# Kernel tuning notes

Hardware: AMD Instinct MI355X
Metric: run time of the kernel (lower is better)

Reference implementation:

```python
import jax, jax.numpy as jnp
import numpy as np

N, E, B = 100000, 3200000, 512
D_IN, D_H, HID = 500, 64, 200
NUM_CLASSES = 80
EPS_BN = 1e-5


def _sage(x, src, dst, Wl, bl, Wr):
    # PyG SAGEConv (mean aggr): out = lin_l(mean_{j->i} x_j) + lin_r(x_i)
    n = x.shape[0]
    agg = jax.ops.segment_sum(x[src], dst, num_segments=n)          # [n, d_in]
    deg = jax.ops.segment_sum(jnp.ones((src.shape[0],), x.dtype), dst, num_segments=n)
    mean = agg / jnp.maximum(deg, 1.0)[:, None]
    return mean @ Wl + bl + x @ Wr


def _bn(c, g, b):
    # BatchNorm1d, training-mode batch statistics (biased var)
    mu = c.mean(0)
    var = c.var(0)
    return (c - mu) / jnp.sqrt(var + EPS_BN) * g + b


def setup_inputs() -> dict:
    key = jax.random.key(0)
    ks = jax.random.split(key, 16)
    p = lambda k, shape: jax.random.normal(k, shape, dtype=jnp.float32) * 0.05
    z = lambda d: jnp.zeros((d,), jnp.float32)
    o = lambda d: jnp.ones((d,), jnp.float32)
    return {
        "x": jax.random.uniform(ks[0], (N, D_IN), dtype=jnp.float32),
        "edge_index": jax.random.randint(ks[1], (2, E), 0, N),
        "batch": jnp.sort(jax.random.randint(ks[2], (N,), 0, B)),
        "y": jax.random.randint(ks[3], (B,), 0, NUM_CLASSES),
        "conv1_Wl": p(ks[4], (D_IN, D_H)), "conv1_bl": z(D_H), "conv1_Wr": p(ks[5], (D_IN, D_H)),
        "conv2_Wl": p(ks[6], (D_H, D_H)),  "conv2_bl": z(D_H), "conv2_Wr": p(ks[7], (D_H, D_H)),
        "conv3_Wl": p(ks[8], (D_H, D_H)),  "conv3_bl": z(D_H), "conv3_Wr": p(ks[9], (D_H, D_H)),
        "lin1_W": p(ks[10], (D_H, HID)), "lin1_b": z(HID),
        "bn1_g": o(HID), "bn1_beta": z(HID),
        "lin2_W": p(ks[11], (HID, HID // 2)), "lin2_b": z(HID // 2),
        "bn2_g": o(HID // 2), "bn2_beta": z(HID // 2),
        "lin3_W": p(ks[12], (HID // 2, HID // 2)), "lin3_b": z(HID // 2),
        "bn3_g": o(HID // 2), "bn3_beta": z(HID // 2),
        "lin4_W": p(ks[13], (HID // 2, NUM_CLASSES)), "lin4_b": z(NUM_CLASSES),
    }


def reference(x, edge_index, batch, y,
              conv1_Wl, conv1_bl, conv1_Wr,
              conv2_Wl, conv2_bl, conv2_Wr,
              conv3_Wl, conv3_bl, conv3_Wr,
              lin1_W, lin1_b, bn1_g, bn1_beta,
              lin2_W, lin2_b, bn2_g, bn2_beta,
              lin3_W, lin3_b, bn3_g, bn3_beta,
              lin4_W, lin4_b):
    src, dst = edge_index[0], edge_index[1]
    # F.normalize(x, p=1.0, dim=-1)
    xn = x / jnp.maximum(jnp.abs(x).sum(-1, keepdims=True), 1e-12)
    e = _sage(xn, src, dst, conv1_Wl, conv1_bl, conv1_Wr)
    e = _sage(e, src, dst, conv2_Wl, conv2_bl, conv2_Wr)
    e = _sage(e, src, dst, conv3_Wl, conv3_bl, conv3_Wr)
    # global_mean_pool over graph ids
    sums = jax.ops.segment_sum(e, batch, num_segments=B)             # [B, 64]
    cnts = jax.ops.segment_sum(jnp.ones((e.shape[0],), e.dtype), batch, num_segments=B)
    c = sums / jnp.maximum(cnts, 1.0)[:, None]
    # dropout (p=0.1) omitted for a deterministic reference
    c = c @ lin1_W + lin1_b
    b = jnp.tanh(_bn(c, bn1_g, bn1_beta))
    c = b @ lin2_W + lin2_b
    b = jnp.tanh(_bn(c, bn2_g, bn2_beta))
    c = b @ lin3_W + lin3_b
    b = jnp.tanh(_bn(c, bn3_g, bn3_beta))
    return b @ lin4_W + lin4_b                                       # [B, 80]
```

## Files before the change

### kernel.cpp

```cpp
#include <hip/hip_runtime.h>
#include <hip/hip_bf16.h>

#define NN 100000
#define NE 3200000
#define NB 512
#define DIN 500
#define DH 64
#define HIDN 200
#define NCLS 80

#define NBUK 256
#define NPB 391
#define EPB 16384
#define NBLK_E ((NE + EPB - 1) / EPB)

typedef __attribute__((ext_vector_type(8))) short bf16x8;
typedef __attribute__((ext_vector_type(4))) float f32x4;

__device__ __forceinline__ short f2bf(float f) {
    union { float f; unsigned u; } v; v.f = f;
    unsigned r = v.u + 0x7FFF + ((v.u >> 16) & 1);
    return (short)(r >> 16);
}
__device__ __forceinline__ float bf2f(short s) {
    union { unsigned u; float f; } v; v.u = ((unsigned)(unsigned short)s) << 16;
    return v.f;
}

__global__ void bukhist_kernel(const int* __restrict__ dst, int* __restrict__ block_hist) {
    __shared__ int h[NBUK];
    for (int i = threadIdx.x; i < NBUK; i += 256) h[i] = 0;
    __syncthreads();
    int base = blockIdx.x * EPB;
    int end = min(base + EPB, NE);
    for (int e = base + threadIdx.x; e < end; e += 256)
        atomicAdd(&h[dst[e] / NPB], 1);
    __syncthreads();
    for (int i = threadIdx.x; i < NBUK; i += 256)
        block_hist[blockIdx.x * NBUK + i] = h[i];
}

__global__ void bukoff_kernel(int* __restrict__ block_hist, int* __restrict__ buk_base) {
    __shared__ int tot[NBUK];
    __shared__ int sc[NBUK];
    int b = threadIdx.x;
    int s = 0;
    for (int i = 0; i < NBLK_E; ++i) s += block_hist[i * NBUK + b];
    tot[b] = s; sc[b] = s;
    __syncthreads();
    for (int o = 1; o < NBUK; o <<= 1) {
        int t = (b >= o) ? sc[b - o] : 0;
        __syncthreads();
        sc[b] += t;
        __syncthreads();
    }
    int excl = sc[b] - tot[b];
    buk_base[b] = excl;
    if (b == NBUK - 1) buk_base[NBUK] = excl + tot[b];
    int run = excl;
    for (int i = 0; i < NBLK_E; ++i) {
        int idx = i * NBUK + b;
        int v = block_hist[idx];
        block_hist[idx] = run;
        run += v;
    }
}

__global__ void bukscat_kernel(const int* __restrict__ src, const int* __restrict__ dst,
                               const int* __restrict__ block_hist, int* __restrict__ bpack) {
    __shared__ int cur[NBUK];
    for (int i = threadIdx.x; i < NBUK; i += 256)
        cur[i] = block_hist[blockIdx.x * NBUK + i];
    __syncthreads();
    int base = blockIdx.x * EPB;
    int end = min(base + EPB, NE);
    for (int e = base + threadIdx.x; e < end; e += 256) {
        int d = dst[e];
        int bk = d / NPB;
        int p = atomicAdd(&cur[bk], 1);
        bpack[p] = (src[e] << 9) | (d - bk * NPB);
    }
}

__global__ void bukfin_kernel(const int* __restrict__ buk_base, const int* __restrict__ bpack,
                              int* __restrict__ row_ptr, float* __restrict__ invdeg,
                              int* __restrict__ csr_src) {
    __shared__ int cnt[NPB];
    __shared__ int cbase[NPB];
    int bk = blockIdx.x;
    int n0 = bk * NPB;
    int nloc = min(n0 + NPB, NN) - n0;
    for (int i = threadIdx.x; i < nloc; i += 256) cnt[i] = 0;
    __syncthreads();
    int beg = buk_base[bk], end = buk_base[bk + 1];
    for (int p = beg + threadIdx.x; p < end; p += 256)
        atomicAdd(&cnt[bpack[p] & 511], 1);
    __syncthreads();
    if (threadIdx.x == 0) {
        int run = beg;
        for (int i = 0; i < nloc; ++i) { int v = cnt[i]; cbase[i] = run; run += v; }
    }
    __syncthreads();
    for (int i = threadIdx.x; i < nloc; i += 256) {
        row_ptr[n0 + i] = cbase[i];
        invdeg[n0 + i] = 1.0f / fmaxf((float)cnt[i], 1.0f);
        cnt[i] = cbase[i];
    }
    if (bk == NBUK - 1 && threadIdx.x == 0) row_ptr[NN] = end;
    __syncthreads();
    for (int p = beg + threadIdx.x; p < end; p += 256) {
        int v = bpack[p];
        int q = atomicAdd(&cnt[v & 511], 1);
        csr_src[q] = v >> 9;
    }
}

__global__ void wprep_frag(const float* __restrict__ Wl, const float* __restrict__ Wr,
                           short* __restrict__ Wf) {
    int id = blockIdx.x * blockDim.x + threadIdx.x;
    if (id >= 16 * 8 * 64) return;
    int l = id & 63;
    int c = (id >> 6) & 7;
    int t = id >> 9;
    int q = l >> 4, r16 = l & 15;
    int col = c * 16 + r16;
    short v[8];
#pragma unroll
    for (int i = 0; i < 8; ++i) {
        int k = t * 32 + q * 8 + i;
        float f = 0.f;
        if (k < DIN) f = (col < 64) ? Wl[(size_t)k * 64 + col] : Wr[(size_t)k * 64 + (col - 64)];
        v[i] = f2bf(f);
    }
    *(bf16x8*)(Wf + (size_t)id * 8) = *(bf16x8*)v;
}

__global__ void wprep64(const float* __restrict__ W, short* __restrict__ Wb) {
    int id = blockIdx.x * blockDim.x + threadIdx.x;
    if (id >= 64 * 64) return;
    int col = id >> 6, k = id & 63;
    Wb[col * 64 + k] = f2bf(W[(size_t)k * 64 + col]);
}

__launch_bounds__(256)
__global__ void gemm_direct2(const float* __restrict__ in, const short* __restrict__ Wf,
                             short* __restrict__ Hl, float* __restrict__ Hr) {
    const int tid = threadIdx.x;
    const int w = tid >> 6, l = tid & 63;
    const int q = l >> 4, r16 = l & 15;
    const int tile0 = blockIdx.x * 64 + w * 16;
    const int arow_i = tile0 + r16;
    const bool ok = arow_i < NN;
    const float* arow = in + (size_t)(ok ? arow_i : 0) * DIN + q * 8;
    const short* wf = Wf + (size_t)l * 8;

    f32x4 acc[8];
#pragma unroll
    for (int c = 0; c < 8; ++c) acc[c] = (f32x4){0.f, 0.f, 0.f, 0.f};
    float pabs = 0.f;

#pragma unroll 2
    for (int t = 0; t < 16; ++t) {
        float v[8];
        if (t < 15) {
            const float4 f0 = *(const float4*)(arow + t * 32);
            const float4 f1 = *(const float4*)(arow + t * 32 + 4);
            v[0] = f0.x; v[1] = f0.y; v[2] = f0.z; v[3] = f0.w;
            v[4] = f1.x; v[5] = f1.y; v[6] = f1.z; v[7] = f1.w;
        } else {
#pragma unroll
            for (int i = 0; i < 8; ++i) {
                int gk = t * 32 + q * 8 + i;
                v[i] = (gk < DIN) ? arow[t * 32 + i] : 0.f;
            }
        }
        short sh[8];
#pragma unroll
        for (int i = 0; i < 8; ++i) { pabs += fabsf(v[i]); sh[i] = f2bf(v[i]); }
        bf16x8 a = *(bf16x8*)sh;
#pragma unroll
        for (int c = 0; c < 8; ++c) {
            bf16x8 b = *(const bf16x8*)(wf + ((size_t)(t * 8 + c) << 9));
            acc[c] = __builtin_amdgcn_mfma_f32_16x16x32_bf16(a, b, acc[c], 0, 0, 0);
        }
    }

    pabs += __shfl_xor(pabs, 16, 64);
    pabs += __shfl_xor(pabs, 32, 64);
    float sval = 1.0f / fmaxf(pabs, 1e-12f);

#pragma unroll
    for (int rr = 0; rr < 4; ++rr) {
        int lrow = q * 4 + rr;
        float srow = __shfl(sval, lrow, 64);
        int grow = tile0 + lrow;
        if (grow < NN) {
#pragma unroll
            for (int c = 0; c < 8; ++c) {
                float o = acc[c][rr] * srow;
                if (c < 4) Hl[(size_t)grow * 64 + c * 16 + r16] = f2bf(o);
                else       Hr[(size_t)grow * 64 + (c - 4) * 16 + r16] = o;
            }
        }
    }
}

__launch_bounds__(256)
__global__ void gather_kernel(const int* __restrict__ row_ptr, const int* __restrict__ csr_src,
                              const short* __restrict__ Hl, const float* __restrict__ Hr,
                              const float* __restrict__ invdeg, const float* __restrict__ bl,
                              short* __restrict__ ebf) {
    int node = blockIdx.x * 4 + (threadIdx.x >> 6);
    if (node >= NN) return;
    int lane = threadIdx.x & 63;
    int ng = lane >> 3;
    int fl = lane & 7;
    int beg = row_ptr[node], end = row_ptr[node + 1];
    float a0[8], a1[8];
#pragma unroll
    for (int j = 0; j < 8; ++j) { a0[j] = 0.f; a1[j] = 0.f; }
    int p = beg + ng;
    for (; p + 8 < end; p += 16) {
        int s0 = csr_src[p];
        int s1 = csr_src[p + 8];
        bf16x8 v0 = *(const bf16x8*)(Hl + (size_t)s0 * 64 + fl * 8);
        bf16x8 v1 = *(const bf16x8*)(Hl + (size_t)s1 * 64 + fl * 8);
#pragma unroll
        for (int j = 0; j < 8; ++j) { a0[j] += bf2f(v0[j]); a1[j] += bf2f(v1[j]); }
    }
    if (p < end) {
        int s0 = csr_src[p];
        bf16x8 v0 = *(const bf16x8*)(Hl + (size_t)s0 * 64 + fl * 8);
#pragma unroll
        for (int j = 0; j < 8; ++j) a0[j] += bf2f(v0[j]);
    }
#pragma unroll
    for (int j = 0; j < 8; ++j) a0[j] += a1[j];
#pragma unroll
    for (int m = 8; m < 64; m <<= 1)
#pragma unroll
        for (int j = 0; j < 8; ++j) a0[j] += __shfl_xor(a0[j], m, 64);
    if (ng == 0) {
        float idg = invdeg[node];
        const float4 h0 = *(const float4*)(Hr + (size_t)node * 64 + fl * 8);
        const float4 h1 = *(const float4*)(Hr + (size_t)node * 64 + fl * 8 + 4);
        short s[8];
        s[0] = f2bf(a0[0] * idg + bl[fl * 8 + 0] + h0.x);
        s[1] = f2bf(a0[1] * idg + bl[fl * 8 + 1] + h0.y);
        s[2] = f2bf(a0[2] * idg + bl[fl * 8 + 2] + h0.z);
        s[3] = f2bf(a0[3] * idg + bl[fl * 8 + 3] + h0.w);
        s[4] = f2bf(a0[4] * idg + bl[fl * 8 + 4] + h1.x);
        s[5] = f2bf(a0[5] * idg + bl[fl * 8 + 5] + h1.y);
        s[6] = f2bf(a0[6] * idg + bl[fl * 8 + 6] + h1.z);
        s[7] = f2bf(a0[7] * idg + bl[fl * 8 + 7] + h1.w);
        *(bf16x8*)(ebf + (size_t)node * 64 + fl * 8) = *(bf16x8*)s;
    }
}

__launch_bounds__(256)
__global__ void gathermean_kernel(const int* __restrict__ row_ptr, const int* __restrict__ csr_src,
                                  const short* __restrict__ ein, const float* __restrict__ invdeg,
                                  short* __restrict__ m) {
    int node = blockIdx.x * 4 + (threadIdx.x >> 6);
    if (node >= NN) return;
    int lane = threadIdx.x & 63;
    int ng = lane >> 3;
    int fl = lane & 7;
    int beg = row_ptr[node], end = row_ptr[node + 1];
    float a0[8], a1[8];
#pragma unroll
    for (int j = 0; j < 8; ++j) { a0[j] = 0.f; a1[j] = 0.f; }
    int p = beg + ng;
    for (; p + 8 < end; p += 16) {
        int s0 = csr_src[p];
        int s1 = csr_src[p + 8];
        bf16x8 v0 = *(const bf16x8*)(ein + (size_t)s0 * 64 + fl * 8);
        bf16x8 v1 = *(const bf16x8*)(ein + (size_t)s1 * 64 + fl * 8);
#pragma unroll
        for (int j = 0; j < 8; ++j) { a0[j] += bf2f(v0[j]); a1[j] += bf2f(v1[j]); }
    }
    if (p < end) {
        int s0 = csr_src[p];
        bf16x8 v0 = *(const bf16x8*)(ein + (size_t)s0 * 64 + fl * 8);
#pragma unroll
        for (int j = 0; j < 8; ++j) a0[j] += bf2f(v0[j]);
    }
#pragma unroll
    for (int j = 0; j < 8; ++j) a0[j] += a1[j];
#pragma unroll
    for (int mm = 8; mm < 64; mm <<= 1)
#pragma unroll
        for (int j = 0; j < 8; ++j) a0[j] += __shfl_xor(a0[j], mm, 64);
    if (ng == 0) {
        float idg = invdeg[node];
        short s[8];
#pragma unroll
        for (int j = 0; j < 8; ++j) s[j] = f2bf(a0[j] * idg);
        *(bf16x8*)(m + (size_t)node * 64 + fl * 8) = *(bf16x8*)s;
    }
}

template<bool LAST>
__launch_bounds__(256)
__global__ void gemm_dual64(const short* __restrict__ m, const short* __restrict__ ein,
                            const short* __restrict__ Wbl, const short* __restrict__ Wbr,
                            const float* __restrict__ bl,
                            short* __restrict__ eout, float* __restrict__ e3out) {
    const int tid = threadIdx.x;
    const int row0 = blockIdx.x * 64;
    const int w = tid >> 6, l = tid & 63;
    const int q = l >> 4, r16 = l & 15;
    const int arow = row0 + w * 16 + r16;
    const bool ok = arow < NN;
    const short* mp = m   + (size_t)(ok ? arow : 0) * 64 + q * 8;
    const short* ep = ein + (size_t)(ok ? arow : 0) * 64 + q * 8;
    f32x4 acc[4];
#pragma unroll
    for (int c = 0; c < 4; ++c) acc[c] = (f32x4){0.f, 0.f, 0.f, 0.f};
    const bf16x8 z8 = (bf16x8){0, 0, 0, 0, 0, 0, 0, 0};
#pragma unroll
    for (int t = 0; t < 2; ++t) {
        bf16x8 am = ok ? *(const bf16x8*)(mp + t * 32) : z8;
        bf16x8 ae = ok ? *(const bf16x8*)(ep + t * 32) : z8;
#pragma unroll
        for (int c = 0; c < 4; ++c) {
            bf16x8 wl = *(const bf16x8*)(Wbl + (size_t)(c * 16 + r16) * 64 + t * 32 + q * 8);
            bf16x8 wr = *(const bf16x8*)(Wbr + (size_t)(c * 16 + r16) * 64 + t * 32 + q * 8);
            acc[c] = __builtin_amdgcn_mfma_f32_16x16x32_bf16(am, wl, acc[c], 0, 0, 0);
            acc[c] = __builtin_amdgcn_mfma_f32_16x16x32_bf16(ae, wr, acc[c], 0, 0, 0);
        }
    }
#pragma unroll
    for (int c = 0; c < 4; ++c) {
#pragma unroll
        for (int rr = 0; rr < 4; ++rr) {
            int grow = row0 + w * 16 + q * 4 + rr;
            int col = c * 16 + r16;
            if (grow < NN) {
                float o = acc[c][rr] + bl[col];
                if (LAST) e3out[(size_t)grow * 64 + col] = o;
                else      eout[(size_t)grow * 64 + col]  = f2bf(o);
            }
        }
    }
}

__global__ void gseg_kernel(const int* __restrict__ batch, int* __restrict__ gstart) {
    int i = blockIdx.x * blockDim.x + threadIdx.x;
    if (i >= NN) return;
    int bc = batch[i];
    int bp = (i == 0) ? -1 : batch[i - 1];
    for (int b = bp + 1; b <= bc; ++b) gstart[b] = i;
    if (i == NN - 1)
        for (int b = bc + 1; b <= NB; ++b) gstart[b] = NN;
}

__launch_bounds__(256)
__global__ void pool_seg(const float* __restrict__ e, const int* __restrict__ gstart,
                         float* __restrict__ c0) {
    __shared__ float part[4][64];
    int b = blockIdx.x;
    int w = threadIdx.x >> 6, lane = threadIdx.x & 63;
    int s = gstart[b], t = gstart[b + 1];
    float acc = 0.f;
    for (int i = s + w; i < t; i += 4) acc += e[(size_t)i * 64 + lane];
    part[w][lane] = acc;
    __syncthreads();
    if (w == 0) {
        float v = part[0][lane] + part[1][lane] + part[2][lane] + part[3][lane];
        c0[b * 64 + lane] = v / fmaxf((float)(t - s), 1.0f);
    }
}

__global__ void lin_kernel(const float* __restrict__ in, const float* __restrict__ W,
                           const float* __restrict__ bias, float* __restrict__ out,
                           int Kd, int Dout) {
    int id = blockIdx.x * blockDim.x + threadIdx.x;
    if (id >= NB * Dout) return;
    int row = id / Dout, col = id - row * Dout;
    const float* ir = in + (size_t)row * Kd;
    float acc = bias[col];
    for (int k = 0; k < Kd; ++k) acc += ir[k] * W[(size_t)k * Dout + col];
    out[id] = acc;
}

__global__ void bnstats_kernel(const float* __restrict__ c, const float* __restrict__ g,
                               const float* __restrict__ beta, float* __restrict__ sa,
                               float* __restrict__ sb, int Dout) {
    int col = blockIdx.x;
    int tid = threadIdx.x;
    float s = 0.f, sq = 0.f;
    for (int r = tid; r < NB; r += 256) {
        float v = c[(size_t)r * Dout + col];
        s += v; sq += v * v;
    }
    __shared__ float ls[256], lq[256];
    ls[tid] = s; lq[tid] = sq;
    __syncthreads();
    for (int o = 128; o > 0; o >>= 1) {
        if (tid < o) { ls[tid] += ls[tid + o]; lq[tid] += lq[tid + o]; }
        __syncthreads();
    }
    if (tid == 0) {
        float mu = ls[0] / NB;
        float var = lq[0] / NB - mu * mu;
        float a = g[col] * rsqrtf(var + 1e-5f);
        sa[col] = a;
        sb[col] = beta[col] - mu * a;
    }
}

__global__ void bnapply_kernel(const float* __restrict__ c, const float* __restrict__ sa,
                               const float* __restrict__ sb, float* __restrict__ bv, int Dout) {
    int id = blockIdx.x * blockDim.x + threadIdx.x;
    if (id >= NB * Dout) return;
    int col = id % Dout;
    bv[id] = tanhf(c[id] * sa[col] + sb[col]);
}

extern "C" void kernel_launch(void* const* d_in, const int* in_sizes, int n_in,
                              void* d_out, int out_size, void* d_ws, size_t ws_size,
                              hipStream_t stream) {
    const float* x    = (const float*)d_in[0];
    const int* ei     = (const int*)d_in[1];
    const int* src    = ei;
    const int* dst    = ei + NE;
    const int* batch  = (const int*)d_in[2];
    const float* c1Wl = (const float*)d_in[4];
    const float* c1bl = (const float*)d_in[5];
    const float* c1Wr = (const float*)d_in[6];
    const float* c2Wl = (const float*)d_in[7];
    const float* c2bl = (const float*)d_in[8];
    const float* c2Wr = (const float*)d_in[9];
    const float* c3Wl = (const float*)d_in[10];
    const float* c3bl = (const float*)d_in[11];
    const float* c3Wr = (const float*)d_in[12];
    const float* l1W  = (const float*)d_in[13]; const float* l1b = (const float*)d_in[14];
    const float* bn1g = (const float*)d_in[15]; const float* bn1b = (const float*)d_in[16];
    const float* l2W  = (const float*)d_in[17]; const float* l2b = (const float*)d_in[18];
    const float* bn2g = (const float*)d_in[19]; const float* bn2b = (const float*)d_in[20];
    const float* l3W  = (const float*)d_in[21]; const float* l3b = (const float*)d_in[22];
    const float* bn3g = (const float*)d_in[23]; const float* bn3b = (const float*)d_in[24];
    const float* l4W  = (const float*)d_in[25]; const float* l4b = (const float*)d_in[26];
    float* out = (float*)d_out;

    char* wsb = (char*)d_ws;
    short* Hl     = (short*)wsb; wsb += (size_t)NN * 64 * 2;
    float* Hr     = (float*)wsb; wsb += (size_t)NN * 64 * 4;
    short* e      = (short*)wsb; wsb += (size_t)NN * 64 * 2;
    short* m      = (short*)wsb; wsb += (size_t)NN * 64 * 2;
    float* e3     = (float*)wsb; wsb += (size_t)NN * 64 * 4;
    float* invdeg = (float*)wsb; wsb += (size_t)NN * 4;
    float* c      = (float*)wsb; wsb += (size_t)NB * HIDN * 4;
    float* bv     = (float*)wsb; wsb += (size_t)NB * HIDN * 4;
    float* sa     = (float*)wsb; wsb += HIDN * 4;
    float* sb     = (float*)wsb; wsb += HIDN * 4;
    short* Wf1    = (short*)wsb; wsb += 16 * 8 * 64 * 8 * 2;
    short* Wb2l   = (short*)wsb; wsb += 64 * 64 * 2;
    short* Wb2r   = (short*)wsb; wsb += 64 * 64 * 2;
    short* Wb3l   = (short*)wsb; wsb += 64 * 64 * 2;
    short* Wb3r   = (short*)wsb; wsb += 64 * 64 * 2;
    int* row_ptr  = (int*)wsb;   wsb += (size_t)(NN + 1) * 4;
    int* csr_src  = (int*)wsb;   wsb += (size_t)NE * 4;
    int* buk_base = (int*)wsb;   wsb += (NBUK + 1) * 4;
    int* gstart   = (int*)wsb;   wsb += (NB + 1) * 4;
    int* bpack      = (int*)Hl;
    int* block_hist = (int*)e;

    bukhist_kernel<<<NBLK_E, 256, 0, stream>>>(dst, block_hist);
    bukoff_kernel<<<1, NBUK, 0, stream>>>(block_hist, buk_base);
    bukscat_kernel<<<NBLK_E, 256, 0, stream>>>(src, dst, block_hist, bpack);
    bukfin_kernel<<<NBUK, 256, 0, stream>>>(buk_base, bpack, row_ptr, invdeg, csr_src);

    gseg_kernel<<<(NN + 255) / 256, 256, 0, stream>>>(batch, gstart);

    wprep_frag<<<(16 * 8 * 64 + 255) / 256, 256, 0, stream>>>(c1Wl, c1Wr, Wf1);
    wprep64<<<(64 * 64 + 255) / 256, 256, 0, stream>>>(c2Wl, Wb2l);
    wprep64<<<(64 * 64 + 255) / 256, 256, 0, stream>>>(c2Wr, Wb2r);
    wprep64<<<(64 * 64 + 255) / 256, 256, 0, stream>>>(c3Wl, Wb3l);
    wprep64<<<(64 * 64 + 255) / 256, 256, 0, stream>>>(c3Wr, Wb3r);

    const int GB64 = (NN + 63) / 64;
    const int GGB  = (NN + 3) / 4;

    gemm_direct2<<<GB64, 256, 0, stream>>>(x, Wf1, Hl, Hr);
    gather_kernel<<<GGB, 256, 0, stream>>>(row_ptr, csr_src, Hl, Hr, invdeg, c1bl, e);
    gathermean_kernel<<<GGB, 256, 0, stream>>>(row_ptr, csr_src, e, invdeg, m);
    gemm_dual64<false><<<GB64, 256, 0, stream>>>(m, e, Wb2l, Wb2r, c2bl, e, nullptr);
    gathermean_kernel<<<GGB, 256, 0, stream>>>(row_ptr, csr_src, e, invdeg, m);
    gemm_dual64<true><<<GB64, 256, 0, stream>>>(m, e, Wb3l, Wb3r, c3bl, nullptr, e3);

    pool_seg<<<NB, 256, 0, stream>>>(e3, gstart, bv);

    lin_kernel<<<(NB * 200 + 255) / 256, 256, 0, stream>>>(bv, l1W, l1b, c, 64, 200);
    bnstats_kernel<<<200, 256, 0, stream>>>(c, bn1g, bn1b, sa, sb, 200);
    bnapply_kernel<<<(NB * 200 + 255) / 256, 256, 0, stream>>>(c, sa, sb, bv, 200);

    lin_kernel<<<(NB * 100 + 255) / 256, 256, 0, stream>>>(bv, l2W, l2b, c, 200, 100);
    bnstats_kernel<<<100, 256, 0, stream>>>(c, bn2g, bn2b, sa, sb, 100);
    bnapply_kernel<<<(NB * 100 + 255) / 256, 256, 0, stream>>>(c, sa, sb, bv, 100);

    lin_kernel<<<(NB * 100 + 255) / 256, 256, 0, stream>>>(bv, l3W, l3b, c, 100, 100);
    bnstats_kernel<<<100, 256, 0, stream>>>(c, bn3g, bn3b, sa, sb, 100);
    bnapply_kernel<<<(NB * 100 + 255) / 256, 256, 0, stream>>>(c, sa, sb, bv, 100);

    lin_kernel<<<(NB * 80 + 255) / 256, 256, 0, stream>>>(bv, l4W, l4b, out, 100, 80);
}
```

Measured before the change: 613.6 us.

## Split first-layer GEMM K dimension across wave pairs with LDS reduction

The first SAGE projection GEMM now splits the 500-wide K dimension in half between two waves per 16-row tile, with each block covering 32 rows instead of 64. The second half's partial accumulators and L1-norm sums are reduced through shared memory before the scaled outputs are written. This halves each wave's serial MFMA/load chain and doubles the block count to expose more memory-level parallelism. In exchange it adds a __syncthreads, LDS traffic, and leaves half the waves idle during the epilogue.

```diff
diff --git a/kernel.cpp b/kernel.cpp
--- a/kernel.cpp
+++ b/kernel.cpp
@@ -143,16 +143,19 @@
 }
 
 __launch_bounds__(256)
-__global__ void gemm_direct2(const float* __restrict__ in, const short* __restrict__ Wf,
-                             short* __restrict__ Hl, float* __restrict__ Hr) {
+__global__ void gemm_splitk(const float* __restrict__ in, const short* __restrict__ Wf,
+                            short* __restrict__ Hl, float* __restrict__ Hr) {
+    __shared__ float red[2][64][36];
     const int tid = threadIdx.x;
     const int w = tid >> 6, l = tid & 63;
+    const int g = w >> 1;
+    const int h = w & 1;
     const int q = l >> 4, r16 = l & 15;
-    const int tile0 = blockIdx.x * 64 + w * 16;
+    const int tile0 = blockIdx.x * 32 + g * 16;
     const int arow_i = tile0 + r16;
     const bool ok = arow_i < NN;
-    const float* arow = in + (size_t)(ok ? arow_i : 0) * DIN + q * 8;
-    const short* wf = Wf + (size_t)l * 8;
+    const float* arow = in + (size_t)(ok ? arow_i : 0) * DIN + h * 256 + q * 8;
+    const short* wf = Wf + (size_t)l * 8 + (size_t)h * 8 * 8 * 512;
 
     f32x4 acc[8];
 #pragma unroll
@@ -160,9 +163,9 @@
     float pabs = 0.f;
 
 #pragma unroll 2
-    for (int t = 0; t < 16; ++t) {
+    for (int t = 0; t < 8; ++t) {
         float v[8];
-        if (t < 15) {
+        if (h == 0 || t < 7) {
             const float4 f0 = *(const float4*)(arow + t * 32);
             const float4 f1 = *(const float4*)(arow + t * 32 + 4);
             v[0] = f0.x; v[1] = f0.y; v[2] = f0.z; v[3] = f0.w;
@@ -170,7 +173,7 @@
         } else {
 #pragma unroll
             for (int i = 0; i < 8; ++i) {
-                int gk = t * 32 + q * 8 + i;
+                int gk = 256 + t * 32 + q * 8 + i;
                 v[i] = (gk < DIN) ? arow[t * 32 + i] : 0.f;
             }
         }
@@ -185,21 +188,34 @@
         }
     }
 
-    pabs += __shfl_xor(pabs, 16, 64);
-    pabs += __shfl_xor(pabs, 32, 64);
-    float sval = 1.0f / fmaxf(pabs, 1e-12f);
-
-#pragma unroll
-    for (int rr = 0; rr < 4; ++rr) {
-        int lrow = q * 4 + rr;
-        float srow = __shfl(sval, lrow, 64);
-        int grow = tile0 + lrow;
-        if (grow < NN) {
-#pragma unroll
-            for (int c = 0; c < 8; ++c) {
-                float o = acc[c][rr] * srow;
-                if (c < 4) Hl[(size_t)grow * 64 + c * 16 + r16] = f2bf(o);
-                else       Hr[(size_t)grow * 64 + (c - 4) * 16 + r16] = o;
+    if (h == 1) {
+#pragma unroll
+        for (int c = 0; c < 8; ++c) *(f32x4*)&red[g][l][c * 4] = acc[c];
+        red[g][l][32] = pabs;
+    }
+    __syncthreads();
+    if (h == 0) {
+#pragma unroll
+        for (int c = 0; c < 8; ++c) {
+            f32x4 o = *(f32x4*)&red[g][l][c * 4];
+            acc[c][0] += o[0]; acc[c][1] += o[1]; acc[c][2] += o[2]; acc[c][3] += o[3];
+        }
+        pabs += red[g][l][32];
+        pabs += __shfl_xor(pabs, 16, 64);
+        pabs += __shfl_xor(pabs, 32, 64);
+        float sval = 1.0f / fmaxf(pabs, 1e-12f);
+#pragma unroll
+        for (int rr = 0; rr < 4; ++rr) {
+            int lrow = q * 4 + rr;
+            float srow = __shfl(sval, lrow, 64);
+            int grow = tile0 + lrow;
+            if (grow < NN) {
+#pragma unroll
+                for (int c = 0; c < 8; ++c) {
+                    float o = acc[c][rr] * srow;
+                    if (c < 4) Hl[(size_t)grow * 64 + c * 16 + r16] = f2bf(o);
+                    else       Hr[(size_t)grow * 64 + (c - 4) * 16 + r16] = o;
+                }
             }
         }
     }
@@ -480,10 +496,11 @@
     wprep64<<<(64 * 64 + 255) / 256, 256, 0, stream>>>(c3Wl, Wb3l);
     wprep64<<<(64 * 64 + 255) / 256, 256, 0, stream>>>(c3Wr, Wb3r);
 
+    const int GB32 = (NN + 31) / 32;
     const int GB64 = (NN + 63) / 64;
     const int GGB  = (NN + 3) / 4;
 
-    gemm_direct2<<<GB64, 256, 0, stream>>>(x, Wf1, Hl, Hr);
+    gemm_splitk<<<GB32, 256, 0, stream>>>(x, Wf1, Hl, Hr);
     gather_kernel<<<GGB, 256, 0, stream>>>(row_ptr, csr_src, Hl, Hr, invdeg, c1bl, e);
     gathermean_kernel<<<GGB, 256, 0, stream>>>(row_ptr, csr_src, e, invdeg, m);
     gemm_dual64<false><<<GB64, 256, 0, stream>>>(m, e, Wb2l, Wb2r, c2bl, e, nullptr);
```

Result: faster. 601.4 us (-2.0%).

## Stage layer-1 weights through double-buffered LDS and software-pipeline input loads

Applied to the files above, without the earlier changes.

The first SAGE GEMM now loads the bf16 weight slice for each K-step cooperatively into a double-buffered LDS tile, and each wave reads its fragments from there. Before, every wave read its fragments straight from global memory. The x row loads for the next K-step are issued before the current MFMAs run, so global latency overlaps with compute. The weight prep kernel now writes a plain column-major padded layout to suit the LDS staging. The cost is LDS usage and a block-wide barrier at every K-step.

```diff
diff --git a/kernel.cpp b/kernel.cpp
--- a/kernel.cpp
+++ b/kernel.cpp
@@ -115,24 +115,14 @@
     }
 }
 
-__global__ void wprep_frag(const float* __restrict__ Wl, const float* __restrict__ Wr,
-                           short* __restrict__ Wf) {
+__global__ void wprep_kernel(const float* __restrict__ Wl, const float* __restrict__ Wr,
+                             short* __restrict__ Wb, int K, int KP) {
     int id = blockIdx.x * blockDim.x + threadIdx.x;
-    if (id >= 16 * 8 * 64) return;
-    int l = id & 63;
-    int c = (id >> 6) & 7;
-    int t = id >> 9;
-    int q = l >> 4, r16 = l & 15;
-    int col = c * 16 + r16;
-    short v[8];
-#pragma unroll
-    for (int i = 0; i < 8; ++i) {
-        int k = t * 32 + q * 8 + i;
-        float f = 0.f;
-        if (k < DIN) f = (col < 64) ? Wl[(size_t)k * 64 + col] : Wr[(size_t)k * 64 + (col - 64)];
-        v[i] = f2bf(f);
-    }
-    *(bf16x8*)(Wf + (size_t)id * 8) = *(bf16x8*)v;
+    if (id >= 128 * KP) return;
+    int col = id / KP, k = id - col * KP;
+    float v = 0.f;
+    if (k < K) v = (col < 64) ? Wl[(size_t)k * 64 + col] : Wr[(size_t)k * 64 + (col - 64)];
+    Wb[(size_t)col * KP + k] = f2bf(v);
 }
 
 __global__ void wprep64(const float* __restrict__ W, short* __restrict__ Wb) {
@@ -143,8 +133,9 @@
 }
 
 __launch_bounds__(256)
-__global__ void gemm_direct2(const float* __restrict__ in, const short* __restrict__ Wf,
-                             short* __restrict__ Hl, float* __restrict__ Hr) {
+__global__ void gemm_hyb(const float* __restrict__ in, const short* __restrict__ Wb,
+                         short* __restrict__ Hl, float* __restrict__ Hr) {
+    __shared__ short B_lds[2][128][40];
     const int tid = threadIdx.x;
     const int w = tid >> 6, l = tid & 63;
     const int q = l >> 4, r16 = l & 15;
@@ -152,38 +143,75 @@
     const int arow_i = tile0 + r16;
     const bool ok = arow_i < NN;
     const float* arow = in + (size_t)(ok ? arow_i : 0) * DIN + q * 8;
-    const short* wf = Wf + (size_t)l * 8;
+    const int sb_col = tid >> 1;
+    const int sb_kh  = (tid & 1) * 16;
+    const short* bsrc = Wb + (size_t)sb_col * 512 + sb_kh;
 
     f32x4 acc[8];
 #pragma unroll
     for (int c = 0; c < 8; ++c) acc[c] = (f32x4){0.f, 0.f, 0.f, 0.f};
     float pabs = 0.f;
-
-#pragma unroll 2
-    for (int t = 0; t < 16; ++t) {
-        float v[8];
-        if (t < 15) {
-            const float4 f0 = *(const float4*)(arow + t * 32);
-            const float4 f1 = *(const float4*)(arow + t * 32 + 4);
-            v[0] = f0.x; v[1] = f0.y; v[2] = f0.z; v[3] = f0.w;
-            v[4] = f1.x; v[5] = f1.y; v[6] = f1.z; v[7] = f1.w;
-        } else {
-#pragma unroll
-            for (int i = 0; i < 8; ++i) {
-                int gk = t * 32 + q * 8 + i;
-                v[i] = (gk < DIN) ? arow[t * 32 + i] : 0.f;
-            }
+    float va0[8], va1[8];
+    bf16x8 vb00, vb01, vb10, vb11;
+
+#define ISSUE(T, S) do { \
+    if ((T) < 15) { \
+        const float4 f0 = *(const float4*)(arow + (T) * 32); \
+        const float4 f1 = *(const float4*)(arow + (T) * 32 + 4); \
+        va##S[0] = f0.x; va##S[1] = f0.y; va##S[2] = f0.z; va##S[3] = f0.w; \
+        va##S[4] = f1.x; va##S[5] = f1.y; va##S[6] = f1.z; va##S[7] = f1.w; \
+    } else { \
+        _Pragma("unroll") \
+        for (int i = 0; i < 8; ++i) { \
+            int gk = (T) * 32 + q * 8 + i; \
+            va##S[i] = (gk < DIN) ? arow[(T) * 32 + i] : 0.f; \
+        } \
+    } \
+    vb##S##0 = *(const bf16x8*)(bsrc + (T) * 32); \
+    vb##S##1 = *(const bf16x8*)(bsrc + (T) * 32 + 8); \
+} while (0)
+
+#define STAGE_B(BUF, S) do { \
+    *(bf16x8*)&B_lds[BUF][sb_col][sb_kh]     = vb##S##0; \
+    *(bf16x8*)&B_lds[BUF][sb_col][sb_kh + 8] = vb##S##1; \
+} while (0)
+
+    ISSUE(0, 0); ISSUE(1, 1);
+    STAGE_B(0, 0);
+    __syncthreads();
+#pragma unroll
+    for (int tt = 0; tt < 8; ++tt) {
+        { short sh[8];
+#pragma unroll
+          for (int i = 0; i < 8; ++i) { pabs += fabsf(va0[i]); sh[i] = f2bf(va0[i]); }
+          bf16x8 a = *(bf16x8*)sh;
+          if (tt * 2 + 2 < 16) ISSUE(tt * 2 + 2, 0);
+#pragma unroll
+          for (int c = 0; c < 8; ++c) {
+              bf16x8 b = *(bf16x8*)&B_lds[0][c * 16 + r16][q * 8];
+              acc[c] = __builtin_amdgcn_mfma_f32_16x16x32_bf16(a, b, acc[c], 0, 0, 0);
+          }
+          STAGE_B(1, 1);
+          __syncthreads();
         }
-        short sh[8];
-#pragma unroll
-        for (int i = 0; i < 8; ++i) { pabs += fabsf(v[i]); sh[i] = f2bf(v[i]); }
-        bf16x8 a = *(bf16x8*)sh;
-#pragma unroll
-        for (int c = 0; c < 8; ++c) {
-            bf16x8 b = *(const bf16x8*)(wf + ((size_t)(t * 8 + c) << 9));
-            acc[c] = __builtin_amdgcn_mfma_f32_16x16x32_bf16(a, b, acc[c], 0, 0, 0);
+        { short sh[8];
+#pragma unroll
+          for (int i = 0; i < 8; ++i) { pabs += fabsf(va1[i]); sh[i] = f2bf(va1[i]); }
+          bf16x8 a = *(bf16x8*)sh;
+          if (tt * 2 + 3 < 16) ISSUE(tt * 2 + 3, 1);
+#pragma unroll
+          for (int c = 0; c < 8; ++c) {
+              bf16x8 b = *(bf16x8*)&B_lds[1][c * 16 + r16][q * 8];
+              acc[c] = __builtin_amdgcn_mfma_f32_16x16x32_bf16(a, b, acc[c], 0, 0, 0);
+          }
+          if (tt < 7) {
+              STAGE_B(0, 0);
+              __syncthreads();
+          }
         }
     }
+#undef ISSUE
+#undef STAGE_B
 
     pabs += __shfl_xor(pabs, 16, 64);
     pabs += __shfl_xor(pabs, 32, 64);
@@ -455,7 +483,7 @@
     float* bv     = (float*)wsb; wsb += (size_t)NB * HIDN * 4;
     float* sa     = (float*)wsb; wsb += HIDN * 4;
     float* sb     = (float*)wsb; wsb += HIDN * 4;
-    short* Wf1    = (short*)wsb; wsb += 16 * 8 * 64 * 8 * 2;
+    short* Wb1    = (short*)wsb; wsb += 128 * 512 * 2;
     short* Wb2l   = (short*)wsb; wsb += 64 * 64 * 2;
     short* Wb2r   = (short*)wsb; wsb += 64 * 64 * 2;
     short* Wb3l   = (short*)wsb; wsb += 64 * 64 * 2;
@@ -474,7 +502,7 @@
 
     gseg_kernel<<<(NN + 255) / 256, 256, 0, stream>>>(batch, gstart);
 
-    wprep_frag<<<(16 * 8 * 64 + 255) / 256, 256, 0, stream>>>(c1Wl, c1Wr, Wf1);
+    wprep_kernel<<<(128 * 512 + 255) / 256, 256, 0, stream>>>(c1Wl, c1Wr, Wb1, DIN, 512);
     wprep64<<<(64 * 64 + 255) / 256, 256, 0, stream>>>(c2Wl, Wb2l);
     wprep64<<<(64 * 64 + 255) / 256, 256, 0, stream>>>(c2Wr, Wb2r);
     wprep64<<<(64 * 64 + 255) / 256, 256, 0, stream>>>(c3Wl, Wb3l);
@@ -483,7 +511,7 @@
     const int GB64 = (NN + 63) / 64;
     const int GGB  = (NN + 3) / 4;
 
-    gemm_direct2<<<GB64, 256, 0, stream>>>(x, Wf1, Hl, Hr);
+    gemm_hyb<<<GB64, 256, 0, stream>>>(x, Wb1, Hl, Hr);
     gather_kernel<<<GGB, 256, 0, stream>>>(row_ptr, csr_src, Hl, Hr, invdeg, c1bl, e);
     gathermean_kernel<<<GGB, 256, 0, stream>>>(row_ptr, csr_src, e, invdeg, m);
     gemm_dual64<false><<<GB64, 256, 0, stream>>>(m, e, Wb2l, Wb2r, c2bl, e, nullptr);
```

Result: slower. 632.9 us (+3.2%).
